# Kernel optimization log

Measured on AMD Instinct MI355X. Metric: run time of the kernel, lower is better.

Reference implementation:

```python
import jax, jax.numpy as jnp
import numpy as np

N = 6144; D0 = 512; D1 = 256; D2 = 128; K = 10
ALPHA = 1.0; BETA = 1.0; P = 0.004  # edge density -> ~25 avg degree


def _xavier(key, shape):
    limit = float(np.sqrt(6.0 / (shape[0] + shape[1])))
    return jax.random.uniform(key, shape, jnp.float32, -limit, limit)


def setup_inputs() -> dict:
    key = jax.random.key(0)
    ks = jax.random.split(key, 20)

    def adj(k):
        k1, k2 = jax.random.split(k)
        u = jax.random.uniform(k1, (N, N), jnp.float32)
        w = jax.random.uniform(k2, (N, N), jnp.float32)
        return jnp.where(u < P, w, 0.0)  # sparse weighted adjacency, dense storage

    return {
        "A": adj(ks[0]), "A2": adj(ks[1]),
        "X": jax.random.normal(ks[2], (N, D0), jnp.float32),
        "X2": jax.random.normal(ks[3], (N, D0), jnp.float32),
        "W11": _xavier(ks[4], (D0, D1)), "v111": _xavier(ks[5], (D1, 1)), "v112": _xavier(ks[6], (D1, 1)),
        "W12": _xavier(ks[7], (D1, D2)), "v121": _xavier(ks[8], (D2, 1)), "v122": _xavier(ks[9], (D2, 1)),
        "W21": _xavier(ks[10], (D0, D1)), "v211": _xavier(ks[11], (D1, 1)), "v212": _xavier(ks[12], (D1, 1)),
        "W22": _xavier(ks[13], (D1, D2)), "v221": _xavier(ks[14], (D2, 1)), "v222": _xavier(ks[15], (D2, 1)),
        "mu": _xavier(ks[16], (K, D2)),
    }


def _gat(A, H, v1, v2):
    # logits_ij = A_ij * (H v1)_i + A_ij * (H v2)_j, support = nonzeros of A;
    # torch.sparse.softmax over each row of sigmoid(logits) restricted to support.
    f1 = H @ v1                       # [N,1]
    f2 = H @ v2                       # [N,1]
    logits = A * f1 + A * f2.T        # [N,N]
    mask = A != 0.0
    e = jnp.where(mask, jnp.exp(jax.nn.sigmoid(logits)), 0.0)
    denom = jnp.sum(e, axis=1, keepdims=True)
    return e / jnp.where(denom == 0.0, 1.0, denom)  # empty rows -> all-zero row


def _autoenc(A, X, layers):
    H = X
    Cs = []
    for (W, v1, v2) in layers:          # encoder
        H = H @ W
        C = _gat(A, H, v1, v2)
        Cs.append(C)
        H = C @ H
    H_enc = H
    for i in range(len(layers) - 1, -1, -1):  # decoder (tied weights, cached attention)
        H = H @ layers[i][0].T
        H = Cs[i] @ H
    return H_enc, H


def reference(A, X, A2, X2, W11, v111, v112, W12, v121, v122,
              W21, v211, v212, W22, v221, v222, mu):
    H, X_ = _autoenc(A, X, [(W11, v111, v112), (W12, v121, v122)])
    H2, X_2 = _autoenc(A2, X2, [(W21, v211, v212), (W22, v221, v222)])
    H_F = H + H2 * BETA
    # Student-t soft assignment
    d2 = jnp.sum((H_F[:, None, :] - mu[None, :, :]) ** 2, axis=2)  # [N,K]
    q = (1.0 / (1.0 + d2 / ALPHA)) ** ((ALPHA + 1.0) / 2.0)
    q = q / jnp.sum(q, axis=1, keepdims=True)
    return (H_F, q, H, H2, X_, X_2)
```

## Files before the change

### kernel.cpp

```cpp
#include <hip/hip_runtime.h>
#include <hip/hip_bf16.h>

#define NN 6144
#define CAP 128

typedef short bf8 __attribute__((ext_vector_type(8)));
typedef float f4 __attribute__((ext_vector_type(4)));

__device__ inline unsigned short f2bf(float x) {
  union { float f; unsigned u; } v; v.f = x;
  unsigned r = v.u + 0x7fff + ((v.u >> 16) & 1);
  return (unsigned short)(r >> 16);
}
__device__ inline float bf2f(unsigned short b) {
  union { float f; unsigned u; } v; v.u = ((unsigned)b) << 16;
  return v.f;
}

__global__ __launch_bounds__(256) void sparsify2_kernel(
    const float* __restrict__ A0, const float* __restrict__ A1,
    int* __restrict__ colsB, float* __restrict__ valsB, int* __restrict__ cntB) {
  const int br = blockIdx.y;
  const float* __restrict__ A = br ? A1 : A0;
  int* cols = colsB + (size_t)br * NN * CAP;
  float* vals = valsB + (size_t)br * NN * CAP;
  int* cnt = cntB + br * NN;
  int row = (blockIdx.x * blockDim.x + threadIdx.x) >> 6;
  int lane = threadIdx.x & 63;
  const f4* __restrict__ arow = (const f4*)(A + (size_t)row * NN);
  int base = 0;
  for (int it = 0; it < 24; it += 6) {
    f4 v[6];
#pragma unroll
    for (int u = 0; u < 6; ++u) v[u] = __builtin_nontemporal_load(&arow[(it + u) * 64 + lane]);
#pragma unroll
    for (int u = 0; u < 6; ++u) {
      float xs[4] = {v[u][0], v[u][1], v[u][2], v[u][3]};
      unsigned long long m[4];
#pragma unroll
      for (int q = 0; q < 4; ++q) m[q] = __ballot(xs[q] != 0.0f);
      int off0 = base;
      int off1 = off0 + __popcll(m[0]);
      int off2 = off1 + __popcll(m[1]);
      int off3 = off2 + __popcll(m[2]);
      base = off3 + __popcll(m[3]);
      int offs[4] = {off0, off1, off2, off3};
      unsigned long long lmask = (1ull << lane) - 1ull;
#pragma unroll
      for (int q = 0; q < 4; ++q) {
        if (xs[q] != 0.0f) {
          int idx = offs[q] + __popcll(m[q] & lmask);
          if (idx < CAP) {
            cols[row * CAP + idx] = ((it + u) * 64 + lane) * 4 + q;
            vals[row * CAP + idx] = xs[q];
          }
        }
      }
    }
  }
  if (lane == 0) cnt[row] = base < CAP ? base : CAP;
}

__global__ __launch_bounds__(256) void convw_all(
    const float* __restrict__ W11, const float* __restrict__ W21,
    const float* __restrict__ W12, const float* __restrict__ W22,
    short* __restrict__ W1h, short* __restrict__ W1l,
    short* __restrict__ W1th, short* __restrict__ W1tl,
    short* __restrict__ W2h, short* __restrict__ W2l,
    short* __restrict__ W2th, short* __restrict__ W2tl) {
  const int S1 = 512 * 256, S2 = 256 * 128;
  int i = blockIdx.x * 256 + threadIdx.x;
  if (i < 2 * S1) {
    int br = i >= S1;
    int idx = br ? i - S1 : i;
    float x = (br ? W21 : W11)[idx];
    unsigned short h = f2bf(x), l = f2bf(x - bf2f(h));
    int r = idx / 256, c = idx % 256;
    size_t o = (size_t)br * S1;
    W1h[o + idx] = (short)h; W1l[o + idx] = (short)l;
    W1th[o + c * 512 + r] = (short)h; W1tl[o + c * 512 + r] = (short)l;
  } else {
    int i2 = i - 2 * S1;
    if (i2 >= 2 * S2) return;
    int br = i2 >= S2;
    int idx = br ? i2 - S2 : i2;
    float x = (br ? W22 : W12)[idx];
    unsigned short h = f2bf(x), l = f2bf(x - bf2f(h));
    int r = idx / 128, c = idx % 128;
    size_t o = (size_t)br * S2;
    W2h[o + idx] = (short)h; W2l[o + idx] = (short)l;
    W2th[o + c * 256 + r] = (short)h; W2tl[o + c * 256 + r] = (short)l;
  }
}

__global__ __launch_bounds__(256) void convX_kernel(
    const float* __restrict__ X0, const float* __restrict__ X1,
    short* __restrict__ XhB) {
  const int br = blockIdx.y;
  const float* __restrict__ in = br ? X1 : X0;
  short* hi = XhB + (size_t)br * NN * 512;
  int i = blockIdx.x * 256 + threadIdx.x;
  float4 v = *(const float4*)&in[i * 4];
  short4 h;
  h.x = (short)f2bf(v.x);
  h.y = (short)f2bf(v.y);
  h.z = (short)f2bf(v.z);
  h.w = (short)f2bf(v.w);
  *(short4*)&hi[i * 4] = h;
}

template <int D>
__global__ __launch_bounds__(256) void fvec_kernel(
    const short* __restrict__ HB, const float* __restrict__ v10,
    const float* __restrict__ v20, const float* __restrict__ v11,
    const float* __restrict__ v21, float* __restrict__ f1B, float* __restrict__ f2B) {
  const int br = blockIdx.y;
  const short* H = HB + (size_t)br * NN * D;
  const float* v1 = br ? v11 : v10;
  const float* v2 = br ? v21 : v20;
  float* f1 = f1B + br * NN;
  float* f2 = f2B + br * NN;
  int row = (blockIdx.x * blockDim.x + threadIdx.x) >> 6;
  int lane = threadIdx.x & 63;
  constexpr int E = D / 64;
  const short* hp = H + (size_t)row * D + lane * E;
  float s1 = 0.f, s2 = 0.f;
#pragma unroll
  for (int e = 0; e < E; ++e) {
    float h = bf2f((unsigned short)hp[e]);
    s1 += h * v1[lane * E + e];
    s2 += h * v2[lane * E + e];
  }
#pragma unroll
  for (int o = 32; o; o >>= 1) {
    s1 += __shfl_xor(s1, o);
    s2 += __shfl_xor(s2, o);
  }
  if (lane == 0) { f1[row] = s1; f2[row] = s2; }
}

template <bool WF32>
__global__ __launch_bounds__(256) void gatspmm_kernel(
    const int* __restrict__ colsB, const float* __restrict__ avalsB,
    const int* __restrict__ cntB, const float* __restrict__ f1B,
    const float* __restrict__ f2B, float* __restrict__ cvalsB,
    const short* __restrict__ HinB, float* __restrict__ HoutB,
    short* __restrict__ HhB) {
  const int br = blockIdx.y;
  const int* cols = colsB + (size_t)br * NN * CAP;
  const float* avals = avalsB + (size_t)br * NN * CAP;
  const int* cnt = cntB + br * NN;
  const float* f1 = f1B + br * NN;
  const float* f2 = f2B + br * NN;
  float* cvals = cvalsB + (size_t)br * NN * CAP;
  const short* Hin = HinB + (size_t)br * NN * 128;
  int row = (blockIdx.x * blockDim.x + threadIdx.x) >> 6;
  int lane = threadIdx.x & 63;
  int c = cnt[row];
  float f1i = f1[row];
  const int base = row * CAP;
  float e0 = 0.f, e1 = 0.f;
  int j0 = 0, j1 = 0;
  {
    int k = lane;
    if (k < c) {
      float a = avals[base + k];
      j0 = cols[base + k];
      float lg = a * (f1i + f2[j0]);
      e0 = expf(1.f / (1.f + expf(-lg)));
    }
    k = 64 + lane;
    if (k < c) {
      float a = avals[base + k];
      j1 = cols[base + k];
      float lg = a * (f1i + f2[j1]);
      e1 = expf(1.f / (1.f + expf(-lg)));
    }
  }
  float s = e0 + e1;
#pragma unroll
  for (int o = 32; o; o >>= 1) s += __shfl_xor(s, o);
  float inv = (s == 0.f) ? 1.f : 1.f / s;
  if (lane < c) cvals[base + lane] = e0 * inv;
  if (64 + lane < c) cvals[base + 64 + lane] = e1 * inv;

  float2 acc = make_float2(0.f, 0.f);
  for (int k = 0; k < c; k += 4) {
    unsigned hv[4]; float cv[4];
#pragma unroll
    for (int u = 0; u < 4; ++u) {
      int kk = k + u;
      if (kk < c) {
        int jj = (kk & 64) ? j1 : j0;
        float ee = (kk & 64) ? e1 : e0;
        int j = __shfl(jj, kk & 63);
        cv[u] = __shfl(ee, kk & 63) * inv;
        hv[u] = *(const unsigned*)&Hin[(size_t)j * 128 + lane * 2];
      }
    }
#pragma unroll
    for (int u = 0; u < 4; ++u) {
      if (k + u < c) {
        acc.x += cv[u] * bf2f((unsigned short)(hv[u] & 0xffff));
        acc.y += cv[u] * bf2f((unsigned short)(hv[u] >> 16));
      }
    }
  }
  size_t o = (size_t)br * NN * 128 + (size_t)row * 128 + lane * 2;
  if constexpr (WF32) *(float2*)&HoutB[o] = acc;
  unsigned hw = (unsigned)(unsigned short)f2bf(acc.x) | ((unsigned)f2bf(acc.y) << 16);
  *(unsigned*)&HhB[o] = hw;
}

__global__ __launch_bounds__(256) void spmm128_kernel(
    const int* __restrict__ colsB, const float* __restrict__ cvalsB,
    const int* __restrict__ cntB, const short* __restrict__ HinB,
    short* __restrict__ HhB) {
  const int br = blockIdx.y;
  const int* cols = colsB + (size_t)br * NN * CAP;
  const float* cvals = cvalsB + (size_t)br * NN * CAP;
  const int* cnt = cntB + br * NN;
  const short* Hin = HinB + (size_t)br * NN * 128;
  int row = (blockIdx.x * blockDim.x + threadIdx.x) >> 6;
  int lane = threadIdx.x & 63;
  int c = cnt[row];
  const int base = row * CAP;
  float cv0 = 0.f, cv1 = 0.f;
  int j0 = 0, j1 = 0;
  if (lane < c) { j0 = cols[base + lane]; cv0 = cvals[base + lane]; }
  if (64 + lane < c) { j1 = cols[base + 64 + lane]; cv1 = cvals[base + 64 + lane]; }
  float2 acc = make_float2(0.f, 0.f);
  for (int k = 0; k < c; k += 4) {
    unsigned hv[4]; float cv[4];
#pragma unroll
    for (int u = 0; u < 4; ++u) {
      int kk = k + u;
      if (kk < c) {
        int jj = (kk & 64) ? j1 : j0;
        float cc = (kk & 64) ? cv1 : cv0;
        int j = __shfl(jj, kk & 63);
        cv[u] = __shfl(cc, kk & 63);
        hv[u] = *(const unsigned*)&Hin[(size_t)j * 128 + lane * 2];
      }
    }
#pragma unroll
    for (int u = 0; u < 4; ++u) {
      if (k + u < c) {
        acc.x += cv[u] * bf2f((unsigned short)(hv[u] & 0xffff));
        acc.y += cv[u] * bf2f((unsigned short)(hv[u] >> 16));
      }
    }
  }
  size_t o = (size_t)br * NN * 128 + (size_t)row * 128 + lane * 2;
  unsigned hw = (unsigned)(unsigned short)f2bf(acc.x) | ((unsigned)f2bf(acc.y) << 16);
  *(unsigned*)&HhB[o] = hw;
}

#define GS 40
#define MFMA_BF16 __builtin_amdgcn_mfma_f32_16x16x32_bf16

template <bool ALO, int EPI>
__global__ __launch_bounds__(256) void gemm_nt(
    const short* __restrict__ AhB, const short* __restrict__ AlB, size_t sA,
    const short* __restrict__ BhB, const short* __restrict__ BlB, size_t sB,
    float* __restrict__ CfB, short* __restrict__ ChB, short* __restrict__ ClB,
    size_t sC, int K, int Nn) {
  __shared__ short sAh[64 * GS], sBh[64 * GS], sBl[64 * GS];
  __shared__ short sAl[ALO ? 64 * GS : 64];
  const int br = blockIdx.z;
  const short* Ahg = AhB + br * sA;
  const short* Bhg = BhB + br * sB;
  const short* Blg = BlB + br * sB;
  const int bm = blockIdx.x * 64, bn = blockIdx.y * 64;
  const int t = threadIdx.x;
  const int lane = t & 63, w = t >> 6;
  const int wm = (w & 1) * 32, wn = (w >> 1) * 32;
  const int fr = lane & 15, fq = lane >> 4;
  const int srow = t >> 2, sk = (t & 3) * 8;

  f4 acc[2][2] = {};

  for (int k0 = 0; k0 < K; k0 += 32) {
    const size_t aoff = (size_t)(bm + srow) * K + k0 + sk;
    const size_t boff = (size_t)(bn + srow) * K + k0 + sk;
    bf8 vah = *(const bf8*)&Ahg[aoff];
    bf8 vbh = *(const bf8*)&Bhg[boff];
    bf8 vbl = *(const bf8*)&Blg[boff];
    bf8 val_;
    if constexpr (ALO) val_ = *(const bf8*)&(AlB + br * sA)[aoff];
    __syncthreads();
    *(bf8*)&sAh[srow * GS + sk] = vah;
    *(bf8*)&sBh[srow * GS + sk] = vbh;
    *(bf8*)&sBl[srow * GS + sk] = vbl;
    if constexpr (ALO) *(bf8*)&sAl[srow * GS + sk] = val_;
    __syncthreads();

    bf8 ah[2], al[2], bh[2], bl[2];
#pragma unroll
    for (int i = 0; i < 2; ++i) {
      ah[i] = *(bf8*)&sAh[(wm + i * 16 + fr) * GS + fq * 8];
      bh[i] = *(bf8*)&sBh[(wn + i * 16 + fr) * GS + fq * 8];
      bl[i] = *(bf8*)&sBl[(wn + i * 16 + fr) * GS + fq * 8];
      if constexpr (ALO) al[i] = *(bf8*)&sAl[(wm + i * 16 + fr) * GS + fq * 8];
    }
#pragma unroll
    for (int mi = 0; mi < 2; ++mi)
#pragma unroll
      for (int ni = 0; ni < 2; ++ni) {
        acc[mi][ni] = MFMA_BF16(ah[mi], bh[ni], acc[mi][ni], 0, 0, 0);
        acc[mi][ni] = MFMA_BF16(ah[mi], bl[ni], acc[mi][ni], 0, 0, 0);
        if constexpr (ALO) acc[mi][ni] = MFMA_BF16(al[mi], bh[ni], acc[mi][ni], 0, 0, 0);
      }
  }

  float* Cf = CfB ? CfB + br * sC : nullptr;
  short* Ch = ChB ? ChB + br * sC : nullptr;
  short* Cl = ClB ? ClB + br * sC : nullptr;
#pragma unroll
  for (int mi = 0; mi < 2; ++mi)
#pragma unroll
    for (int ni = 0; ni < 2; ++ni) {
      int cidx = bn + wn + ni * 16 + fr;
#pragma unroll
      for (int r = 0; r < 4; ++r) {
        size_t off = (size_t)(bm + wm + mi * 16 + fq * 4 + r) * Nn + cidx;
        float x = acc[mi][ni][r];
        if constexpr (EPI == 0) Cf[off] = x;
        if constexpr (EPI >= 1) {
          unsigned short h = f2bf(x);
          Ch[off] = (short)h;
          if constexpr (EPI == 2) Cl[off] = (short)f2bf(x - bf2f(h));
        }
      }
    }
}

__global__ __launch_bounds__(256) void final_kernel(
    const float* __restrict__ H1e, const float* __restrict__ H2e,
    const float* __restrict__ mu, float* __restrict__ hf_out,
    float* __restrict__ q_out) {
  int row = (blockIdx.x * blockDim.x + threadIdx.x) >> 6;
  int lane = threadIdx.x & 63;
  float2 h1 = *(const float2*)&H1e[row * 128 + lane * 2];
  float2 h2 = *(const float2*)&H2e[row * 128 + lane * 2];
  float2 hf = make_float2(h1.x + h2.x, h1.y + h2.y);
  *(float2*)&hf_out[row * 128 + lane * 2] = hf;
  float d2[10];
#pragma unroll
  for (int k = 0; k < 10; ++k) {
    float dx = hf.x - mu[k * 128 + lane * 2];
    float dy = hf.y - mu[k * 128 + lane * 2 + 1];
    d2[k] = dx * dx + dy * dy;
  }
#pragma unroll
  for (int k = 0; k < 10; ++k)
#pragma unroll
    for (int o = 32; o; o >>= 1) d2[k] += __shfl_xor(d2[k], o);
  float q[10], s = 0.f;
#pragma unroll
  for (int k = 0; k < 10; ++k) { q[k] = 1.f / (1.f + d2[k]); s += q[k]; }
  float inv = 1.f / s;
  if (lane < 10) q_out[row * 10 + lane] = q[lane] * inv;
}

extern "C" void kernel_launch(void* const* d_in, const int* in_sizes, int n_in,
                              void* d_out, int out_size, void* d_ws, size_t ws_size,
                              hipStream_t stream) {
  const int D0 = 512, D1 = 256, D2 = 128;
  const int S1 = D0 * D1, S2 = D1 * D2;
  float* out = (float*)d_out;
  const size_t o0 = 0;
  const size_t o1 = o0 + (size_t)NN * 128;
  const size_t o2 = o1 + (size_t)NN * 10;
  const size_t o3 = o2 + (size_t)NN * 128;
  const size_t o4 = o3 + (size_t)NN * 128;
  const size_t o5 = o4 + (size_t)NN * 512;

  char* w = (char*)d_ws;
  auto alloc = [&](size_t bytes) -> void* {
    void* p = (void*)w;
    w += (bytes + 255) & ~(size_t)255;
    return p;
  };
  int*   cols  = (int*)  alloc((size_t)2 * NN * CAP * 4);
  float* avals = (float*)alloc((size_t)2 * NN * CAP * 4);
  float* c1v   = (float*)alloc((size_t)2 * NN * CAP * 4);
  float* c2v   = (float*)alloc((size_t)2 * NN * CAP * 4);
  int*   cnt   = (int*)  alloc((size_t)2 * NN * 4);
  float* f1    = (float*)alloc((size_t)2 * NN * 4);
  float* f2    = (float*)alloc((size_t)2 * NN * 4);
  short* Xh    = (short*)alloc((size_t)2 * NN * D0 * 2);
  short* H1h   = (short*)alloc((size_t)2 * NN * D1 * 2);
  short* G1h   = (short*)alloc((size_t)2 * NN * D2 * 2);
  short* H2h   = (short*)alloc((size_t)2 * NN * D2 * 2);
  short* Hech  = (short*)alloc((size_t)2 * NN * D2 * 2);
  short* C2sh  = (short*)alloc((size_t)2 * NN * D2 * 2);
  short* Cth   = (short*)alloc((size_t)2 * NN * D2 * 2);
  short* Uh    = (short*)alloc((size_t)2 * NN * D1 * 2);
  short* Ul    = (short*)alloc((size_t)2 * NN * D1 * 2);
  short* W1h   = (short*)alloc((size_t)2 * S1 * 2);
  short* W1l   = (short*)alloc((size_t)2 * S1 * 2);
  short* W1th  = (short*)alloc((size_t)2 * S1 * 2);
  short* W1tl  = (short*)alloc((size_t)2 * S1 * 2);
  short* W2h   = (short*)alloc((size_t)2 * S2 * 2);
  short* W2l   = (short*)alloc((size_t)2 * S2 * 2);
  short* W2th  = (short*)alloc((size_t)2 * S2 * 2);
  short* W2tl  = (short*)alloc((size_t)2 * S2 * 2);

  const float* A   = (const float*)d_in[0];
  const float* A2  = (const float*)d_in[1];
  const float* X   = (const float*)d_in[2];
  const float* X2  = (const float*)d_in[3];
  const float* W11 = (const float*)d_in[4];
  const float* v111= (const float*)d_in[5];
  const float* v112= (const float*)d_in[6];
  const float* W12 = (const float*)d_in[7];
  const float* v121= (const float*)d_in[8];
  const float* v122= (const float*)d_in[9];
  const float* W21 = (const float*)d_in[10];
  const float* v211= (const float*)d_in[11];
  const float* v212= (const float*)d_in[12];
  const float* W22 = (const float*)d_in[13];
  const float* v221= (const float*)d_in[14];
  const float* v222= (const float*)d_in[15];
  const float* mu  = (const float*)d_in[16];

  const dim3 rows2(NN / 4, 2);

  convw_all<<<(2 * S1 + 2 * S2) / 256, 256, 0, stream>>>(
      W11, W21, W12, W22, W1h, W1l, W1th, W1tl, W2h, W2l, W2th, W2tl);
  sparsify2_kernel<<<rows2, 256, 0, stream>>>(A, A2, cols, avals, cnt);
  convX_kernel<<<dim3(NN * D0 / 4 / 256, 2), 256, 0, stream>>>(X, X2, Xh);
  gemm_nt<false, 1><<<dim3(NN / 64, D1 / 64, 2), 256, 0, stream>>>(
      Xh, nullptr, (size_t)NN * D0, W1th, W1tl, (size_t)S1,
      nullptr, H1h, nullptr, (size_t)NN * D1, D0, D1);
  fvec_kernel<256><<<rows2, 256, 0, stream>>>(H1h, v111, v112, v211, v212, f1, f2);
  gemm_nt<false, 1><<<dim3(NN / 64, D2 / 64, 2), 256, 0, stream>>>(
      H1h, nullptr, (size_t)NN * D1, W2th, W2tl, (size_t)S2,
      nullptr, G1h, nullptr, (size_t)NN * D2, D1, D2);
  gatspmm_kernel<false><<<rows2, 256, 0, stream>>>(
      cols, avals, cnt, f1, f2, c1v, G1h, nullptr, H2h);
  fvec_kernel<128><<<rows2, 256, 0, stream>>>(H2h, v121, v122, v221, v222, f1, f2);
  gatspmm_kernel<true><<<rows2, 256, 0, stream>>>(
      cols, avals, cnt, f1, f2, c2v, H2h, out + o2, Hech);
  spmm128_kernel<<<rows2, 256, 0, stream>>>(cols, c2v, cnt, Hech, C2sh);
  spmm128_kernel<<<rows2, 256, 0, stream>>>(cols, c1v, cnt, C2sh, Cth);
  gemm_nt<false, 2><<<dim3(NN / 64, D1 / 64, 2), 256, 0, stream>>>(
      Cth, nullptr, (size_t)NN * D2, W2h, W2l, (size_t)S2,
      nullptr, Uh, Ul, (size_t)NN * D1, D2, D1);
  gemm_nt<true, 0><<<dim3(NN / 64, D0 / 64, 2), 256, 0, stream>>>(
      Uh, Ul, (size_t)NN * D1, W1h, W1l, (size_t)S1,
      out + o4, nullptr, nullptr, (size_t)NN * D0, D1, D0);
  final_kernel<<<NN / 4, 256, 0, stream>>>(out + o2, out + o3, mu, out + o0, out + o1);
}
```

Baseline: 188.7 us.

## Merge independent kernels into combined launches and fuse fvec into GAT SpMM epilogue

Independent stages are merged into shared launches that dispatch on block index: sparsify, weight conversion and X conversion in one launch; the second GEMM with the first fvec; the first decoder SpMM with the final soft-assignment kernel. The second fvec pass is folded into the first GAT SpMM epilogue, which computes the attention projections from the fp32 accumulator and writes them to new g1/g2 buffers. This removes several launches and one re-read of H2h, at the cost of heterogeneous blocks sharing a launch and larger register or LDS footprints. The fused projection uses fp32 rather than bf16-rounded values, a small numerical change.

```diff
diff --git a/kernel.cpp b/kernel.cpp
--- a/kernel.cpp
+++ b/kernel.cpp
@@ -17,16 +17,18 @@
   return v.f;
 }
 
-__global__ __launch_bounds__(256) void sparsify2_kernel(
+
+__device__ void dev_sparsify(int bid, int tid,
     const float* __restrict__ A0, const float* __restrict__ A1,
     int* __restrict__ colsB, float* __restrict__ valsB, int* __restrict__ cntB) {
-  const int br = blockIdx.y;
+  const int br = bid >= 1536;
+  const int bb = br ? bid - 1536 : bid;
   const float* __restrict__ A = br ? A1 : A0;
   int* cols = colsB + (size_t)br * NN * CAP;
   float* vals = valsB + (size_t)br * NN * CAP;
   int* cnt = cntB + br * NN;
-  int row = (blockIdx.x * blockDim.x + threadIdx.x) >> 6;
-  int lane = threadIdx.x & 63;
+  int row = (bb * 256 + tid) >> 6;
+  int lane = tid & 63;
   const f4* __restrict__ arow = (const f4*)(A + (size_t)row * NN);
   int base = 0;
   for (int it = 0; it < 24; it += 6) {
@@ -61,7 +63,7 @@
   if (lane == 0) cnt[row] = base < CAP ? base : CAP;
 }
 
-__global__ __launch_bounds__(256) void convw_all(
+__device__ void dev_convw(int cb, int tid,
     const float* __restrict__ W11, const float* __restrict__ W21,
     const float* __restrict__ W12, const float* __restrict__ W22,
     short* __restrict__ W1h, short* __restrict__ W1l,
@@ -69,7 +71,7 @@
     short* __restrict__ W2h, short* __restrict__ W2l,
     short* __restrict__ W2th, short* __restrict__ W2tl) {
   const int S1 = 512 * 256, S2 = 256 * 128;
-  int i = blockIdx.x * 256 + threadIdx.x;
+  int i = cb * 256 + tid;
   if (i < 2 * S1) {
     int br = i >= S1;
     int idx = br ? i - S1 : i;
@@ -93,13 +95,14 @@
   }
 }
 
-__global__ __launch_bounds__(256) void convX_kernel(
+__device__ void dev_convX(int xb, int tid,
     const float* __restrict__ X0, const float* __restrict__ X1,
     short* __restrict__ XhB) {
-  const int br = blockIdx.y;
+  const int br = xb >= 3072;
+  const int b = br ? xb - 3072 : xb;
   const float* __restrict__ in = br ? X1 : X0;
   short* hi = XhB + (size_t)br * NN * 512;
-  int i = blockIdx.x * 256 + threadIdx.x;
+  int i = b * 256 + tid;
   float4 v = *(const float4*)&in[i * 4];
   short4 h;
   h.x = (short)f2bf(v.x);
@@ -109,27 +112,26 @@
   *(short4*)&hi[i * 4] = h;
 }
 
-template <int D>
-__global__ __launch_bounds__(256) void fvec_kernel(
+__device__ void dev_fvec256(int fb, int tid,
     const short* __restrict__ HB, const float* __restrict__ v10,
     const float* __restrict__ v20, const float* __restrict__ v11,
     const float* __restrict__ v21, float* __restrict__ f1B, float* __restrict__ f2B) {
-  const int br = blockIdx.y;
-  const short* H = HB + (size_t)br * NN * D;
+  const int br = fb >= 1536;
+  const int bb = br ? fb - 1536 : fb;
+  const short* H = HB + (size_t)br * NN * 256;
   const float* v1 = br ? v11 : v10;
   const float* v2 = br ? v21 : v20;
   float* f1 = f1B + br * NN;
   float* f2 = f2B + br * NN;
-  int row = (blockIdx.x * blockDim.x + threadIdx.x) >> 6;
-  int lane = threadIdx.x & 63;
-  constexpr int E = D / 64;
-  const short* hp = H + (size_t)row * D + lane * E;
+  int row = (bb * 256 + tid) >> 6;
+  int lane = tid & 63;
+  const short* hp = H + (size_t)row * 256 + lane * 4;
   float s1 = 0.f, s2 = 0.f;
 #pragma unroll
-  for (int e = 0; e < E; ++e) {
+  for (int e = 0; e < 4; ++e) {
     float h = bf2f((unsigned short)hp[e]);
-    s1 += h * v1[lane * E + e];
-    s2 += h * v2[lane * E + e];
+    s1 += h * v1[lane * 4 + e];
+    s2 += h * v2[lane * 4 + e];
   }
 #pragma unroll
   for (int o = 32; o; o >>= 1) {
@@ -139,13 +141,206 @@
   if (lane == 0) { f1[row] = s1; f2[row] = s2; }
 }
 
-template <bool WF32>
+#define GS 40
+#define MFMA_BF16 __builtin_amdgcn_mfma_f32_16x16x32_bf16
+
+template <bool ALO, int EPI>
+__device__ void dev_gemm(int bx, int by, int br, int tid,
+    const short* __restrict__ AhB, const short* __restrict__ AlB, size_t sA,
+    const short* __restrict__ BhB, const short* __restrict__ BlB, size_t sB,
+    float* __restrict__ CfB, short* __restrict__ ChB, short* __restrict__ ClB,
+    size_t sC, int K, int Nn) {
+  __shared__ short sAh[64 * GS], sBh[64 * GS], sBl[64 * GS];
+  __shared__ short sAl[ALO ? 64 * GS : 64];
+  const short* Ahg = AhB + br * sA;
+  const short* Bhg = BhB + br * sB;
+  const short* Blg = BlB + br * sB;
+  const int bm = bx * 64, bn = by * 64;
+  const int t = tid;
+  const int lane = t & 63, w = t >> 6;
+  const int wm = (w & 1) * 32, wn = (w >> 1) * 32;
+  const int fr = lane & 15, fq = lane >> 4;
+  const int srow = t >> 2, sk = (t & 3) * 8;
+
+  f4 acc[2][2] = {};
+
+  for (int k0 = 0; k0 < K; k0 += 32) {
+    const size_t aoff = (size_t)(bm + srow) * K + k0 + sk;
+    const size_t boff = (size_t)(bn + srow) * K + k0 + sk;
+    bf8 vah = *(const bf8*)&Ahg[aoff];
+    bf8 vbh = *(const bf8*)&Bhg[boff];
+    bf8 vbl = *(const bf8*)&Blg[boff];
+    bf8 val_;
+    if constexpr (ALO) val_ = *(const bf8*)&(AlB + br * sA)[aoff];
+    __syncthreads();
+    *(bf8*)&sAh[srow * GS + sk] = vah;
+    *(bf8*)&sBh[srow * GS + sk] = vbh;
+    *(bf8*)&sBl[srow * GS + sk] = vbl;
+    if constexpr (ALO) *(bf8*)&sAl[srow * GS + sk] = val_;
+    __syncthreads();
+
+    bf8 ah[2], al[2], bh[2], bl[2];
+#pragma unroll
+    for (int i = 0; i < 2; ++i) {
+      ah[i] = *(bf8*)&sAh[(wm + i * 16 + fr) * GS + fq * 8];
+      bh[i] = *(bf8*)&sBh[(wn + i * 16 + fr) * GS + fq * 8];
+      bl[i] = *(bf8*)&sBl[(wn + i * 16 + fr) * GS + fq * 8];
+      if constexpr (ALO) al[i] = *(bf8*)&sAl[(wm + i * 16 + fr) * GS + fq * 8];
+    }
+#pragma unroll
+    for (int mi = 0; mi < 2; ++mi)
+#pragma unroll
+      for (int ni = 0; ni < 2; ++ni) {
+        acc[mi][ni] = MFMA_BF16(ah[mi], bh[ni], acc[mi][ni], 0, 0, 0);
+        acc[mi][ni] = MFMA_BF16(ah[mi], bl[ni], acc[mi][ni], 0, 0, 0);
+        if constexpr (ALO) acc[mi][ni] = MFMA_BF16(al[mi], bh[ni], acc[mi][ni], 0, 0, 0);
+      }
+  }
+
+  float* Cf = CfB ? CfB + br * sC : nullptr;
+  short* Ch = ChB ? ChB + br * sC : nullptr;
+  short* Cl = ClB ? ClB + br * sC : nullptr;
+#pragma unroll
+  for (int mi = 0; mi < 2; ++mi)
+#pragma unroll
+    for (int ni = 0; ni < 2; ++ni) {
+      int cidx = bn + wn + ni * 16 + fr;
+#pragma unroll
+      for (int r = 0; r < 4; ++r) {
+        size_t off = (size_t)(bm + wm + mi * 16 + fq * 4 + r) * Nn + cidx;
+        float x = acc[mi][ni][r];
+        if constexpr (EPI == 0) Cf[off] = x;
+        if constexpr (EPI >= 1) {
+          unsigned short h = f2bf(x);
+          Ch[off] = (short)h;
+          if constexpr (EPI == 2) Cl[off] = (short)f2bf(x - bf2f(h));
+        }
+      }
+    }
+}
+
+__device__ void dev_spmm128(int sb, int tid,
+    const int* __restrict__ colsB, const float* __restrict__ cvalsB,
+    const int* __restrict__ cntB, const short* __restrict__ HinB,
+    short* __restrict__ HhB) {
+  const int br = sb >= 1536;
+  const int bb = br ? sb - 1536 : sb;
+  const int* cols = colsB + (size_t)br * NN * CAP;
+  const float* cvals = cvalsB + (size_t)br * NN * CAP;
+  const int* cnt = cntB + br * NN;
+  const short* Hin = HinB + (size_t)br * NN * 128;
+  int row = (bb * 256 + tid) >> 6;
+  int lane = tid & 63;
+  int c = cnt[row];
+  const int base = row * CAP;
+  float cv0 = 0.f, cv1 = 0.f;
+  int j0 = 0, j1 = 0;
+  if (lane < c) { j0 = cols[base + lane]; cv0 = cvals[base + lane]; }
+  if (64 + lane < c) { j1 = cols[base + 64 + lane]; cv1 = cvals[base + 64 + lane]; }
+  float2 acc = make_float2(0.f, 0.f);
+  for (int k = 0; k < c; k += 4) {
+    unsigned hv[4]; float cv[4];
+#pragma unroll
+    for (int u = 0; u < 4; ++u) {
+      int kk = k + u;
+      if (kk < c) {
+        int jj = (kk & 64) ? j1 : j0;
+        float cc = (kk & 64) ? cv1 : cv0;
+        int j = __shfl(jj, kk & 63);
+        cv[u] = __shfl(cc, kk & 63);
+        hv[u] = *(const unsigned*)&Hin[(size_t)j * 128 + lane * 2];
+      }
+    }
+#pragma unroll
+    for (int u = 0; u < 4; ++u) {
+      if (k + u < c) {
+        acc.x += cv[u] * bf2f((unsigned short)(hv[u] & 0xffff));
+        acc.y += cv[u] * bf2f((unsigned short)(hv[u] >> 16));
+      }
+    }
+  }
+  size_t o = (size_t)br * NN * 128 + (size_t)row * 128 + lane * 2;
+  unsigned hw = (unsigned)(unsigned short)f2bf(acc.x) | ((unsigned)f2bf(acc.y) << 16);
+  *(unsigned*)&HhB[o] = hw;
+}
+
+__device__ void dev_final(int fb, int tid,
+    const float* __restrict__ H1e, const float* __restrict__ H2e,
+    const float* __restrict__ mu, float* __restrict__ hf_out,
+    float* __restrict__ q_out) {
+  int row = (fb * 256 + tid) >> 6;
+  int lane = tid & 63;
+  float2 h1 = *(const float2*)&H1e[row * 128 + lane * 2];
+  float2 h2 = *(const float2*)&H2e[row * 128 + lane * 2];
+  float2 hf = make_float2(h1.x + h2.x, h1.y + h2.y);
+  *(float2*)&hf_out[row * 128 + lane * 2] = hf;
+  float d2[10];
+#pragma unroll
+  for (int k = 0; k < 10; ++k) {
+    float dx = hf.x - mu[k * 128 + lane * 2];
+    float dy = hf.y - mu[k * 128 + lane * 2 + 1];
+    d2[k] = dx * dx + dy * dy;
+  }
+#pragma unroll
+  for (int k = 0; k < 10; ++k)
+#pragma unroll
+    for (int o = 32; o; o >>= 1) d2[k] += __shfl_xor(d2[k], o);
+  float q[10], s = 0.f;
+#pragma unroll
+  for (int k = 0; k < 10; ++k) { q[k] = 1.f / (1.f + d2[k]); s += q[k]; }
+  float inv = 1.f / s;
+  if (lane < 10) q_out[row * 10 + lane] = q[lane] * inv;
+}
+
+
+__global__ __launch_bounds__(256) void k1_prep(
+    const float* A0, const float* A1, int* colsB, float* valsB, int* cntB,
+    const float* W11, const float* W21, const float* W12, const float* W22,
+    short* W1h, short* W1l, short* W1th, short* W1tl,
+    short* W2h, short* W2l, short* W2th, short* W2tl,
+    const float* X0, const float* X1, short* XhB) {
+  int bid = blockIdx.x, tid = threadIdx.x;
+  if (bid < 3072) dev_sparsify(bid, tid, A0, A1, colsB, valsB, cntB);
+  else if (bid < 4352) dev_convw(bid - 3072, tid, W11, W21, W12, W22,
+                                 W1h, W1l, W1th, W1tl, W2h, W2l, W2th, W2tl);
+  else dev_convX(bid - 4352, tid, X0, X1, XhB);
+}
+
+template <bool ALO, int EPI>
+__global__ __launch_bounds__(256) void gemm_nt(
+    const short* AhB, const short* AlB, size_t sA,
+    const short* BhB, const short* BlB, size_t sB,
+    float* CfB, short* ChB, short* ClB, size_t sC, int K, int Nn) {
+  dev_gemm<ALO, EPI>(blockIdx.x, blockIdx.y, blockIdx.z, threadIdx.x,
+                     AhB, AlB, sA, BhB, BlB, sB, CfB, ChB, ClB, sC, K, Nn);
+}
+
+__global__ __launch_bounds__(256) void k3_gemm2_fvec(
+    const short* H1h, const short* W2th, const short* W2tl, short* G1h,
+    const float* v111, const float* v112, const float* v211, const float* v212,
+    float* f1, float* f2) {
+  int bid = blockIdx.x, tid = threadIdx.x;
+  if (bid < 384) {
+    int bx = bid % 96, r = bid / 96;
+    int by = r & 1, br = r >> 1;
+    dev_gemm<false, 1>(bx, by, br, tid, H1h, nullptr, (size_t)NN * 256,
+                       W2th, W2tl, (size_t)256 * 128, nullptr, G1h, nullptr,
+                       (size_t)NN * 128, 256, 128);
+  } else {
+    dev_fvec256(bid - 384, tid, H1h, v111, v112, v211, v212, f1, f2);
+  }
+}
+
+template <bool WF32, bool FUSE>
 __global__ __launch_bounds__(256) void gatspmm_kernel(
     const int* __restrict__ colsB, const float* __restrict__ avalsB,
     const int* __restrict__ cntB, const float* __restrict__ f1B,
     const float* __restrict__ f2B, float* __restrict__ cvalsB,
     const short* __restrict__ HinB, float* __restrict__ HoutB,
-    short* __restrict__ HhB) {
+    short* __restrict__ HhB,
+    const float* __restrict__ nv10, const float* __restrict__ nv20,
+    const float* __restrict__ nv11, const float* __restrict__ nv21,
+    float* __restrict__ g1B, float* __restrict__ g2B) {
   const int br = blockIdx.y;
   const int* cols = colsB + (size_t)br * NN * CAP;
   const float* avals = avalsB + (size_t)br * NN * CAP;
@@ -210,157 +405,34 @@
   if constexpr (WF32) *(float2*)&HoutB[o] = acc;
   unsigned hw = (unsigned)(unsigned short)f2bf(acc.x) | ((unsigned)f2bf(acc.y) << 16);
   *(unsigned*)&HhB[o] = hw;
+  if constexpr (FUSE) {
+    const float* w1 = br ? nv11 : nv10;
+    const float* w2 = br ? nv21 : nv20;
+    float s1 = acc.x * w1[lane * 2] + acc.y * w1[lane * 2 + 1];
+    float s2 = acc.x * w2[lane * 2] + acc.y * w2[lane * 2 + 1];
+#pragma unroll
+    for (int o2 = 32; o2; o2 >>= 1) {
+      s1 += __shfl_xor(s1, o2);
+      s2 += __shfl_xor(s2, o2);
+    }
+    if (lane == 0) { g1B[br * NN + row] = s1; g2B[br * NN + row] = s2; }
+  }
+}
+
+__global__ __launch_bounds__(256) void k6_spmm_final(
+    const int* colsB, const float* c2v, const int* cntB,
+    const short* Hech, short* C2sh,
+    const float* H1e, const float* H2e, const float* mu,
+    float* hf_out, float* q_out) {
+  int bid = blockIdx.x, tid = threadIdx.x;
+  if (bid < 3072) dev_spmm128(bid, tid, colsB, c2v, cntB, Hech, C2sh);
+  else dev_final(bid - 3072, tid, H1e, H2e, mu, hf_out, q_out);
 }
 
 __global__ __launch_bounds__(256) void spmm128_kernel(
-    const int* __restrict__ colsB, const float* __restrict__ cvalsB,
-    const int* __restrict__ cntB, const short* __restrict__ HinB,
-    short* __restrict__ HhB) {
-  const int br = blockIdx.y;
-  const int* cols = colsB + (size_t)br * NN * CAP;
-  const float* cvals = cvalsB + (size_t)br * NN * CAP;
-  const int* cnt = cntB + br * NN;
-  const short* Hin = HinB + (size_t)br * NN * 128;
-  int row = (blockIdx.x * blockDim.x + threadIdx.x) >> 6;
-  int lane = threadIdx.x & 63;
-  int c = cnt[row];
-  const int base = row * CAP;
-  float cv0 = 0.f, cv1 = 0.f;
-  int j0 = 0, j1 = 0;
-  if (lane < c) { j0 = cols[base + lane]; cv0 = cvals[base + lane]; }
-  if (64 + lane < c) { j1 = cols[base + 64 + lane]; cv1 = cvals[base + 64 + lane]; }
-  float2 acc = make_float2(0.f, 0.f);
-  for (int k = 0; k < c; k += 4) {
-    unsigned hv[4]; float cv[4];
-#pragma unroll
-    for (int u = 0; u < 4; ++u) {
-      int kk = k + u;
-      if (kk < c) {
-        int jj = (kk & 64) ? j1 : j0;
-        float cc = (kk & 64) ? cv1 : cv0;
-        int j = __shfl(jj, kk & 63);
-        cv[u] = __shfl(cc, kk & 63);
-        hv[u] = *(const unsigned*)&Hin[(size_t)j * 128 + lane * 2];
-      }
-    }
-#pragma unroll
-    for (int u = 0; u < 4; ++u) {
-      if (k + u < c) {
-        acc.x += cv[u] * bf2f((unsigned short)(hv[u] & 0xffff));
-        acc.y += cv[u] * bf2f((unsigned short)(hv[u] >> 16));
-      }
-    }
-  }
-  size_t o = (size_t)br * NN * 128 + (size_t)row * 128 + lane * 2;
-  unsigned hw = (unsigned)(unsigned short)f2bf(acc.x) | ((unsigned)f2bf(acc.y) << 16);
-  *(unsigned*)&HhB[o] = hw;
-}
-
-#define GS 40
-#define MFMA_BF16 __builtin_amdgcn_mfma_f32_16x16x32_bf16
-
-template <bool ALO, int EPI>
-__global__ __launch_bounds__(256) void gemm_nt(
-    const short* __restrict__ AhB, const short* __restrict__ AlB, size_t sA,
-    const short* __restrict__ BhB, const short* __restrict__ BlB, size_t sB,
-    float* __restrict__ CfB, short* __restrict__ ChB, short* __restrict__ ClB,
-    size_t sC, int K, int Nn) {
-  __shared__ short sAh[64 * GS], sBh[64 * GS], sBl[64 * GS];
-  __shared__ short sAl[ALO ? 64 * GS : 64];
-  const int br = blockIdx.z;
-  const short* Ahg = AhB + br * sA;
-  const short* Bhg = BhB + br * sB;
-  const short* Blg = BlB + br * sB;
-  const int bm = blockIdx.x * 64, bn = blockIdx.y * 64;
-  const int t = threadIdx.x;
-  const int lane = t & 63, w = t >> 6;
-  const int wm = (w & 1) * 32, wn = (w >> 1) * 32;
-  const int fr = lane & 15, fq = lane >> 4;
-  const int srow = t >> 2, sk = (t & 3) * 8;
-
-  f4 acc[2][2] = {};
-
-  for (int k0 = 0; k0 < K; k0 += 32) {
-    const size_t aoff = (size_t)(bm + srow) * K + k0 + sk;
-    const size_t boff = (size_t)(bn + srow) * K + k0 + sk;
-    bf8 vah = *(const bf8*)&Ahg[aoff];
-    bf8 vbh = *(const bf8*)&Bhg[boff];
-    bf8 vbl = *(const bf8*)&Blg[boff];
-    bf8 val_;
-    if constexpr (ALO) val_ = *(const bf8*)&(AlB + br * sA)[aoff];
-    __syncthreads();
-    *(bf8*)&sAh[srow * GS + sk] = vah;
-    *(bf8*)&sBh[srow * GS + sk] = vbh;
-    *(bf8*)&sBl[srow * GS + sk] = vbl;
-    if constexpr (ALO) *(bf8*)&sAl[srow * GS + sk] = val_;
-    __syncthreads();
-
-    bf8 ah[2], al[2], bh[2], bl[2];
-#pragma unroll
-    for (int i = 0; i < 2; ++i) {
-      ah[i] = *(bf8*)&sAh[(wm + i * 16 + fr) * GS + fq * 8];
-      bh[i] = *(bf8*)&sBh[(wn + i * 16 + fr) * GS + fq * 8];
-      bl[i] = *(bf8*)&sBl[(wn + i * 16 + fr) * GS + fq * 8];
-      if constexpr (ALO) al[i] = *(bf8*)&sAl[(wm + i * 16 + fr) * GS + fq * 8];
-    }
-#pragma unroll
-    for (int mi = 0; mi < 2; ++mi)
-#pragma unroll
-      for (int ni = 0; ni < 2; ++ni) {
-        acc[mi][ni] = MFMA_BF16(ah[mi], bh[ni], acc[mi][ni], 0, 0, 0);
-        acc[mi][ni] = MFMA_BF16(ah[mi], bl[ni], acc[mi][ni], 0, 0, 0);
-        if constexpr (ALO) acc[mi][ni] = MFMA_BF16(al[mi], bh[ni], acc[mi][ni], 0, 0, 0);
-      }
-  }
-
-  float* Cf = CfB ? CfB + br * sC : nullptr;
-  short* Ch = ChB ? ChB + br * sC : nullptr;
-  short* Cl = ClB ? ClB + br * sC : nullptr;
-#pragma unroll
-  for (int mi = 0; mi < 2; ++mi)
-#pragma unroll
-    for (int ni = 0; ni < 2; ++ni) {
-      int cidx = bn + wn + ni * 16 + fr;
-#pragma unroll
-      for (int r = 0; r < 4; ++r) {
-        size_t off = (size_t)(bm + wm + mi * 16 + fq * 4 + r) * Nn + cidx;
-        float x = acc[mi][ni][r];
-        if constexpr (EPI == 0) Cf[off] = x;
-        if constexpr (EPI >= 1) {
-          unsigned short h = f2bf(x);
-          Ch[off] = (short)h;
-          if constexpr (EPI == 2) Cl[off] = (short)f2bf(x - bf2f(h));
-        }
-      }
-    }
-}
-
-__global__ __launch_bounds__(256) void final_kernel(
-    const float* __restrict__ H1e, const float* __restrict__ H2e,
-    const float* __restrict__ mu, float* __restrict__ hf_out,
-    float* __restrict__ q_out) {
-  int row = (blockIdx.x * blockDim.x + threadIdx.x) >> 6;
-  int lane = threadIdx.x & 63;
-  float2 h1 = *(const float2*)&H1e[row * 128 + lane * 2];
-  float2 h2 = *(const float2*)&H2e[row * 128 + lane * 2];
-  float2 hf = make_float2(h1.x + h2.x, h1.y + h2.y);
-  *(float2*)&hf_out[row * 128 + lane * 2] = hf;
-  float d2[10];
-#pragma unroll
-  for (int k = 0; k < 10; ++k) {
-    float dx = hf.x - mu[k * 128 + lane * 2];
-    float dy = hf.y - mu[k * 128 + lane * 2 + 1];
-    d2[k] = dx * dx + dy * dy;
-  }
-#pragma unroll
-  for (int k = 0; k < 10; ++k)
-#pragma unroll
-    for (int o = 32; o; o >>= 1) d2[k] += __shfl_xor(d2[k], o);
-  float q[10], s = 0.f;
-#pragma unroll
-  for (int k = 0; k < 10; ++k) { q[k] = 1.f / (1.f + d2[k]); s += q[k]; }
-  float inv = 1.f / s;
-  if (lane < 10) q_out[row * 10 + lane] = q[lane] * inv;
+    const int* colsB, const float* cvalsB, const int* cntB,
+    const short* HinB, short* HhB) {
+  dev_spmm128(blockIdx.x + blockIdx.y * 1536, threadIdx.x, colsB, cvalsB, cntB, HinB, HhB);
 }
 
 extern "C" void kernel_launch(void* const* d_in, const int* in_sizes, int n_in,
@@ -389,6 +461,8 @@
   int*   cnt   = (int*)  alloc((size_t)2 * NN * 4);
   float* f1    = (float*)alloc((size_t)2 * NN * 4);
   float* f2    = (float*)alloc((size_t)2 * NN * 4);
+  float* g1    = (float*)alloc((size_t)2 * NN * 4);
+  float* g2    = (float*)alloc((size_t)2 * NN * 4);
   short* Xh    = (short*)alloc((size_t)2 * NN * D0 * 2);
   short* H1h   = (short*)alloc((size_t)2 * NN * D1 * 2);
   short* G1h   = (short*)alloc((size_t)2 * NN * D2 * 2);
@@ -427,23 +501,22 @@
 
   const dim3 rows2(NN / 4, 2);
 
-  convw_all<<<(2 * S1 + 2 * S2) / 256, 256, 0, stream>>>(
-      W11, W21, W12, W22, W1h, W1l, W1th, W1tl, W2h, W2l, W2th, W2tl);
-  sparsify2_kernel<<<rows2, 256, 0, stream>>>(A, A2, cols, avals, cnt);
-  convX_kernel<<<dim3(NN * D0 / 4 / 256, 2), 256, 0, stream>>>(X, X2, Xh);
+  k1_prep<<<10496, 256, 0, stream>>>(
+      A, A2, cols, avals, cnt, W11, W21, W12, W22,
+      W1h, W1l, W1th, W1tl, W2h, W2l, W2th, W2tl, X, X2, Xh);
   gemm_nt<false, 1><<<dim3(NN / 64, D1 / 64, 2), 256, 0, stream>>>(
       Xh, nullptr, (size_t)NN * D0, W1th, W1tl, (size_t)S1,
       nullptr, H1h, nullptr, (size_t)NN * D1, D0, D1);
-  fvec_kernel<256><<<rows2, 256, 0, stream>>>(H1h, v111, v112, v211, v212, f1, f2);
-  gemm_nt<false, 1><<<dim3(NN / 64, D2 / 64, 2), 256, 0, stream>>>(
-      H1h, nullptr, (size_t)NN * D1, W2th, W2tl, (size_t)S2,
-      nullptr, G1h, nullptr, (size_t)NN * D2, D1, D2);
-  gatspmm_kernel<false><<<rows2, 256, 0, stream>>>(
-      cols, avals, cnt, f1, f2, c1v, G1h, nullptr, H2h);
-  fvec_kernel<128><<<rows2, 256, 0, stream>>>(H2h, v121, v122, v221, v222, f1, f2);
-  gatspmm_kernel<true><<<rows2, 256, 0, stream>>>(
-      cols, avals, cnt, f1, f2, c2v, H2h, out + o2, Hech);
-  spmm128_kernel<<<rows2, 256, 0, stream>>>(cols, c2v, cnt, Hech, C2sh);
+  k3_gemm2_fvec<<<3456, 256, 0, stream>>>(
+      H1h, W2th, W2tl, G1h, v111, v112, v211, v212, f1, f2);
+  gatspmm_kernel<false, true><<<rows2, 256, 0, stream>>>(
+      cols, avals, cnt, f1, f2, c1v, G1h, nullptr, H2h,
+      v121, v122, v221, v222, g1, g2);
+  gatspmm_kernel<true, false><<<rows2, 256, 0, stream>>>(
+      cols, avals, cnt, g1, g2, c2v, H2h, out + o2, Hech,
+      nullptr, nullptr, nullptr, nullptr, nullptr, nullptr);
+  k6_spmm_final<<<4608, 256, 0, stream>>>(
+      cols, c2v, cnt, Hech, C2sh, out + o2, out + o3, mu, out + o0, out + o1);
   spmm128_kernel<<<rows2, 256, 0, stream>>>(cols, c1v, cnt, C2sh, Cth);
   gemm_nt<false, 2><<<dim3(NN / 64, D1 / 64, 2), 256, 0, stream>>>(
       Cth, nullptr, (size_t)NN * D2, W2h, W2l, (size_t)S2,
@@ -451,5 +524,4 @@
   gemm_nt<true, 0><<<dim3(NN / 64, D0 / 64, 2), 256, 0, stream>>>(
       Uh, Ul, (size_t)NN * D1, W1h, W1l, (size_t)S1,
       out + o4, nullptr, nullptr, (size_t)NN * D0, D1, D0);
-  final_kernel<<<NN / 4, 256, 0, stream>>>(out + o2, out + o3, mu, out + o0, out + o1);
-}
+}
```

New measurement: 170.8 us. 9.5% less time.
